# Optimization experiments

Measured on AMD Instinct MI355X. Metric: run time of the kernel, lower is better.

Reference implementation:

```python
import jax, jax.numpy as jnp
import numpy as np

HEADS = 16
DIM_HEAD = 64
NONCAUSAL_ATTN_LEN = 64


def setup_inputs() -> dict:
    key = jax.random.key(0)
    k1, k2, k3 = jax.random.split(key, 3)
    b, n, d = 2, 2048, 1024
    inner = HEADS * DIM_HEAD
    x = jax.random.normal(k1, (b, n, d), dtype=jnp.float32)
    mask = jnp.ones((b, n), dtype=bool)
    w_qkv = jax.random.normal(k2, (d, 3 * inner), dtype=jnp.float32) * 0.02
    w_out = jax.random.normal(k3, (inner, d), dtype=jnp.float32) * 0.02
    b_out = jnp.zeros((d,), dtype=jnp.float32)
    return {"x": x, "mask": mask, "w_qkv": w_qkv, "w_out": w_out, "b_out": b_out}


def reference(x, mask, w_qkv, w_out, b_out):
    b, n, _ = x.shape
    h, dh = HEADS, DIM_HEAD
    scale = dh ** -0.5
    qkv = x @ w_qkv                                  # [b, n, 3*h*dh]
    q, k, v = jnp.split(qkv, 3, axis=-1)
    # 'b n (h d) -> b h n d'
    reshape = lambda t: t.reshape(b, n, h, dh).transpose(0, 2, 1, 3)
    q, k, v = reshape(q), reshape(k), reshape(v)
    dots = jnp.einsum('bhid,bhjd->bhij', q, k) * scale  # [b,h,n,n]
    neg = -jnp.finfo(dots.dtype).max
    # padding mask: attend only where both query and key positions are valid
    pm = mask[:, None, :, None] & mask[:, None, None, :]
    dots = jnp.where(~pm, neg, dots)
    # causal mask (strict upper triangle), with noncausal prefix block unmasked
    cm = jnp.triu(jnp.ones((n, n), dtype=bool), k=1)
    L = NONCAUSAL_ATTN_LEN
    if L > 1:
        cm = cm.at[:L, :L].set(False)
    dots = jnp.where(cm, neg, dots)
    attn = jax.nn.softmax(dots, axis=-1)
    out = jnp.einsum('bhij,bhjd->bhid', attn, v)     # [b,h,n,dh]
    out = out.transpose(0, 2, 1, 3).reshape(b, n, h * dh)  # 'b h n d -> b n (h d)'
    return out @ w_out + b_out
```

## Files before the change

kernel.cpp:

```cpp
#include <hip/hip_runtime.h>

typedef __bf16 bf16x8 __attribute__((ext_vector_type(8)));
typedef __bf16 bf16x4 __attribute__((ext_vector_type(4)));
typedef float  f32x4  __attribute__((ext_vector_type(4)));

#define SC2 0.18033688011112042f

__device__ __forceinline__ void gload16(const void* g, void* l) {
    __builtin_amdgcn_global_load_lds(
        (const __attribute__((address_space(1))) unsigned int*)g,
        (__attribute__((address_space(3))) unsigned int*)l, 16, 0, 0);
}

__device__ __forceinline__ float max3f(float a, float b, float c) {
    return fmaxf(fmaxf(a, b), c);
}

__global__ __launch_bounds__(256) void prep_k(
    const float* __restrict__ x, const float* __restrict__ w_qkv,
    const float* __restrict__ w_out, __bf16* __restrict__ xb,
    __bf16* __restrict__ wqkvT, __bf16* __restrict__ woutT)
{
    __shared__ float tile[32][33];
    const int blk = blockIdx.x, tid = threadIdx.x;
    if (blk < 4096) {
        int i = blk * 256 + tid;
        float4 v = ((const float4*)x)[i];
        bf16x4 o;
        o[0] = (__bf16)v.x; o[1] = (__bf16)v.y; o[2] = (__bf16)v.z; o[3] = (__bf16)v.w;
        ((bf16x4*)xb)[i] = o;
        return;
    }
    const float* in; __bf16* outp; int C, t0;
    if (blk < 7168) { in = w_qkv; outp = wqkvT; C = 3072; t0 = blk - 4096; }
    else            { in = w_out; outp = woutT; C = 1024; t0 = blk - 7168; }
    const int R = 1024;
    const int tpr = C >> 5;
    const int c0 = (t0 % tpr) * 32, r0 = (t0 / tpr) * 32;
    const int tx = tid & 31, ty = tid >> 5;
#pragma unroll
    for (int p = 0; p < 4; ++p)
        tile[ty + p * 8][tx] = in[(size_t)(r0 + ty + p * 8) * C + c0 + tx];
    __syncthreads();
#pragma unroll
    for (int p = 0; p < 4; ++p)
        outp[(size_t)(c0 + ty + p * 8) * R + r0 + tx] = (__bf16)tile[tx][ty + p * 8];
}

template<int MODE, int BM>
__global__ __launch_bounds__(256) void gemm_bf16_k(
    const __bf16* __restrict__ A, const __bf16* __restrict__ Bt,
    void* __restrict__ Cout, const float* __restrict__ bias,
    int M, int N, int K)
{
    constexpr int MI = BM / 32;
    __shared__ __bf16 As[2][BM * 32];
    __shared__ __bf16 Bs[2][128 * 32];
    const int tid = threadIdx.x;
    const int m0 = blockIdx.x * BM, n0 = blockIdx.y * 128;
    const int wave = tid >> 6, lane = tid & 63;
    const int lr = lane & 15, lk = lane >> 4;

    const int row4 = lane >> 2;
    const int sg   = (lane & 3) ^ (row4 & 3);

    const int wm = (BM == 128) ? (wave >> 1) * 64 : (wave & 1) * 32;
    const int wn = (BM == 128) ? (wave & 1) * 64 : (wave >> 1) * 64;

    f32x4 acc[MI][4] = {};

    auto stage = [&](int k0, int bufi) {
        if (BM == 128) {
#pragma unroll
            for (int c = 0; c < 2; ++c) {
                int row = c * 64 + wave * 16 + row4;
                gload16(A + (size_t)(m0 + row) * K + k0 + sg * 8,
                        (char*)&As[bufi][0] + c * 4096 + wave * 1024);
            }
        } else {
            int row = wave * 16 + row4;
            gload16(A + (size_t)(m0 + row) * K + k0 + sg * 8,
                    (char*)&As[bufi][0] + wave * 1024);
        }
#pragma unroll
        for (int c = 0; c < 2; ++c) {
            int row = c * 64 + wave * 16 + row4;
            gload16(Bt + (size_t)(n0 + row) * K + k0 + sg * 8,
                    (char*)&Bs[bufi][0] + c * 4096 + wave * 1024);
        }
    };

    const int nsteps = K >> 5;
    stage(0, 0);
    for (int s = 0; s < nsteps; ++s) {
        __syncthreads();
        if (s + 1 < nsteps) stage((s + 1) * 32, (s + 1) & 1);
        const int bufi = s & 1;

        bf16x8 af[MI], bfr[4];
#pragma unroll
        for (int i = 0; i < MI; ++i) {
            int row = wm + i * 16 + lr;
            af[i]  = *(const bf16x8*)((char*)&As[bufi][0] + row * 64 +
                                      ((lk ^ (row & 3)) << 4));
        }
#pragma unroll
        for (int j = 0; j < 4; ++j) {
            int row = wn + j * 16 + lr;
            bfr[j] = *(const bf16x8*)((char*)&Bs[bufi][0] + row * 64 +
                                      ((lk ^ (row & 3)) << 4));
        }
        __builtin_amdgcn_s_setprio(1);
#pragma unroll
        for (int i = 0; i < MI; ++i)
#pragma unroll
            for (int j = 0; j < 4; ++j)
                acc[i][j] = __builtin_amdgcn_mfma_f32_16x16x32_bf16(
                    af[i], bfr[j], acc[i][j], 0, 0, 0);
        __builtin_amdgcn_s_setprio(0);
    }

#pragma unroll
    for (int i = 0; i < MI; ++i) {
#pragma unroll
        for (int j = 0; j < 4; ++j) {
            int row0 = m0 + wm + i * 16 + lk * 4;
            int col  = n0 + wn + j * 16 + lr;
            if (MODE == 0) {
                int which = col >> 10, rem = col & 1023;
                int h = rem >> 6, dh = rem & 63;
                int bb = row0 >> 11, nn0 = row0 & 2047;
                if (which == 2) {
                    bf16x4 o;
#pragma unroll
                    for (int r = 0; r < 4; ++r) o[r] = (__bf16)acc[i][j][r];
                    size_t off = (size_t)8388608 +
                                 (((size_t)bb * 16 + h) * 64 + dh) * 2048 + nn0;
                    *(bf16x4*)((__bf16*)Cout + off) = o;
                } else {
                    float sc = (which == 0) ? SC2 : 1.f;
#pragma unroll
                    for (int r = 0; r < 4; ++r) {
                        size_t off = ((((size_t)which * 2 + bb) * 16 + h) * 2048
                                      + nn0 + r) * 64 + dh;
                        ((__bf16*)Cout)[off] = (__bf16)(acc[i][j][r] * sc);
                    }
                }
            } else {
#pragma unroll
                for (int r = 0; r < 4; ++r)
                    ((float*)Cout)[(size_t)(row0 + r) * N + col] =
                        acc[i][j][r] + bias[col];
            }
        }
    }
}

__global__ __launch_bounds__(256) void flash_attn_k(
    const __bf16* __restrict__ qkv, __bf16* __restrict__ out)
{
    __shared__ __bf16 Ks[2][64 * 64];
    __shared__ __bf16 Vt[2][64 * 64];
    __shared__ __bf16 Ps[4 * 16 * 64];

    const int g = blockIdx.x;
    const int xcd = g & 7, i = g >> 3;
    const int bh = xcd + 8 * (i & 3);
    const int qp = i >> 2;
    const int qtA = qp, qtB = 31 - qp;
    const int b = bh >> 4, h = bh & 15;
    const int wave = threadIdx.x >> 6, lane = threadIdx.x & 63;
    const int lr = lane & 15, lk = lane >> 4;

    const size_t headoff = ((size_t)b * 16 + h) * 2048 * 64;
    const __bf16* Qp  = qkv + headoff;
    const __bf16* Kp  = qkv + (size_t)4194304 + headoff;
    const __bf16* Vtp = qkv + (size_t)8388608 + headoff;

    const int row8 = lane >> 3;
    const int sg   = (lane & 7) ^ row8;

    bf16x8 qfA[2], qfB[2];
    {
        const __bf16* qa = Qp + (size_t)(qtA * 64 + wave * 16 + lr) * 64 + lk * 8;
        qfA[0] = *(const bf16x8*)(qa);
        qfA[1] = *(const bf16x8*)(qa + 32);
        const __bf16* qb = Qp + (size_t)(qtB * 64 + wave * 16 + lr) * 64 + lk * 8;
        qfB[0] = *(const bf16x8*)(qb);
        qfB[1] = *(const bf16x8*)(qb + 32);
    }

    bf16x8 ones;
#pragma unroll
    for (int j = 0; j < 8; ++j) ones[j] = (__bf16)1.0f;

    float mA = 0.f, mB = 0.f;
    f32x4 lAacc = {}, lBacc = {};
    f32x4 oA[4] = {}, oB[4] = {};

    char* PsW = (char*)Ps + wave * 2048;

    auto stage = [&](int t, int bufi) {
        const int j0 = t * 64;
#pragma unroll
        for (int c = 0; c < 2; ++c) {
            int row = c * 32 + wave * 8 + row8;
            gload16(Kp + (size_t)(j0 + row) * 64 + sg * 8,
                    (char*)&Ks[bufi][0] + c * 4096 + wave * 1024);
            gload16(Vtp + (size_t)row * 2048 + j0 + sg * 8,
                    (char*)&Vt[bufi][0] + c * 4096 + wave * 1024);
        }
    };

    auto process = [&](int bufi, const bf16x8 (&qf)[2], float& m, f32x4& lacc,
                       f32x4 (&acc_o)[4], bool diag) {
        const float nm = -m;
        f32x4 sacc[4];
#pragma unroll
        for (int nf = 0; nf < 4; ++nf) sacc[nf] = f32x4{nm, nm, nm, nm};
        __builtin_amdgcn_s_setprio(1);
#pragma unroll
        for (int nf = 0; nf < 4; ++nf) {
            int arow = nf * 16 + lr;
#pragma unroll
            for (int ks = 0; ks < 2; ++ks) {
                int kb = (arow * 128 + (ks * 32 + lk * 8) * 2) ^ ((arow & 7) << 4);
                bf16x8 kf = *(const bf16x8*)((char*)&Ks[bufi][0] + kb);
                sacc[nf] = __builtin_amdgcn_mfma_f32_16x16x32_bf16(
                    kf, qf[ks], sacc[nf], 0, 0, 0);
            }
        }
        __builtin_amdgcn_s_setprio(0);
        if (diag) {
#pragma unroll
            for (int nf = 0; nf < 4; ++nf)
#pragma unroll
                for (int r = 0; r < 4; ++r)
                    if (nf * 16 + lk * 4 + r > wave * 16 + lr)
                        sacc[nf][r] = -1e30f;
        }
        float t0 = max3f(sacc[0][0], sacc[0][1], sacc[0][2]);
        float t1 = max3f(sacc[0][3], sacc[1][0], sacc[1][1]);
        float t2 = max3f(sacc[1][2], sacc[1][3], sacc[2][0]);
        float t3 = max3f(sacc[2][1], sacc[2][2], sacc[2][3]);
        float t4 = max3f(sacc[3][0], sacc[3][1], sacc[3][2]);
        float v = fmaxf(max3f(max3f(t0, t1, t2), t3, t4), sacc[3][3]);
        v = fmaxf(v, __shfl_xor(v, 16));
        v = fmaxf(v, __shfl_xor(v, 32));
        if (__builtin_expect(__any(v > 8.f), 0)) {
            float vc = fmaxf(v, 0.f);
            float alpha = exp2f(-vc);
            m += vc;
            float a_r[4];
#pragma unroll
            for (int r = 0; r < 4; ++r) a_r[r] = __shfl(alpha, lk * 4 + r);
#pragma unroll
            for (int r = 0; r < 4; ++r) lacc[r] *= a_r[r];
#pragma unroll
            for (int nf = 0; nf < 4; ++nf)
#pragma unroll
                for (int r = 0; r < 4; ++r) {
                    acc_o[nf][r] *= a_r[r];
                    sacc[nf][r] -= vc;
                }
        }
#pragma unroll
        for (int nf = 0; nf < 4; ++nf) {
            bf16x4 o;
#pragma unroll
            for (int r = 0; r < 4; ++r) o[r] = (__bf16)exp2f(sacc[nf][r]);
            int pb = (lr * 128 + nf * 32 + lk * 8) ^ ((lr & 7) << 4);
            *(bf16x4*)(PsW + pb) = o;
        }
        __builtin_amdgcn_s_setprio(1);
#pragma unroll
        for (int ks = 0; ks < 2; ++ks) {
            int pb = (lr * 128 + ks * 64 + lk * 16) ^ ((lr & 7) << 4);
            bf16x8 pa = *(const bf16x8*)(PsW + pb);
            lacc = __builtin_amdgcn_mfma_f32_16x16x32_bf16(pa, ones, lacc, 0, 0, 0);
#pragma unroll
            for (int nf = 0; nf < 4; ++nf) {
                int d = nf * 16 + lr;
                int vb = (d * 128 + ks * 64 + lk * 16) ^ ((d & 7) << 4);
                bf16x8 vf = *(const bf16x8*)((char*)&Vt[bufi][0] + vb);
                acc_o[nf] = __builtin_amdgcn_mfma_f32_16x16x32_bf16(
                    pa, vf, acc_o[nf], 0, 0, 0);
            }
        }
        __builtin_amdgcn_s_setprio(0);
    };

    const int nt = qtB + 1;
    stage(0, 0);
    for (int t = 0; t < nt; ++t) {
        __syncthreads();
        if (t + 1 < nt) stage(t + 1, (t + 1) & 1);
        if (t <= qtA) process(t & 1, qfA, mA, lAacc, oA, t == qtA && qtA > 0);
        process(t & 1, qfB, mB, lBacc, oB, t == qtB);
    }

    float lAr[4], lBr[4];
#pragma unroll
    for (int r = 0; r < 4; ++r) {
        lAr[r] = 1.f / lAacc[r];
        lBr[r] = 1.f / lBacc[r];
    }
    const int rowbase = (b << 11) + wave * 16 + lk * 4;
    const int colbase = h * 64 + lr;
#pragma unroll
    for (int nf = 0; nf < 4; ++nf)
#pragma unroll
        for (int r = 0; r < 4; ++r) {
            out[(size_t)(rowbase + qtA * 64 + r) * 1024 + colbase + nf * 16] =
                (__bf16)(oA[nf][r] * lAr[r]);
            out[(size_t)(rowbase + qtB * 64 + r) * 1024 + colbase + nf * 16] =
                (__bf16)(oB[nf][r] * lBr[r]);
        }
}

extern "C" void kernel_launch(void* const* d_in, const int* in_sizes, int n_in,
                              void* d_out, int out_size, void* d_ws, size_t ws_size,
                              hipStream_t stream)
{
    const float* x     = (const float*)d_in[0];
    const float* w_qkv = (const float*)d_in[2];
    const float* w_out = (const float*)d_in[3];
    const float* b_out = (const float*)d_in[4];

    char* ws = (char*)d_ws;
    __bf16* xb    = (__bf16*)(ws);
    __bf16* wqkvT = (__bf16*)(ws + 8388608);
    __bf16* woutT = (__bf16*)(ws + 14680064);
    __bf16* qkvp  = (__bf16*)(ws + 16777216);
    __bf16* aout  = (__bf16*)(ws + 41943040);

    prep_k<<<8192, 256, 0, stream>>>(x, w_qkv, w_out, xb, wqkvT, woutT);

    gemm_bf16_k<0, 128><<<dim3(32, 24), 256, 0, stream>>>(
        xb, wqkvT, (void*)qkvp, nullptr, 4096, 3072, 1024);
    flash_attn_k<<<512, 256, 0, stream>>>(qkvp, aout);
    gemm_bf16_k<1, 64><<<dim3(64, 8), 256, 0, stream>>>(
        aout, woutT, (void*)d_out, b_out, 4096, 1024, 1024);
}
```

Measured before the change: 113.1 us.

## Rewrite flash attention with 32x32 MFMA, 2-wave blocks, one query tile each

The attention kernel moves from 16x16x32 to 32x32x16 bf16 MFMA, with each of two waves owning 32 query rows. Blocks shrink from 256 to 128 threads, and each block now handles a single query tile instead of a paired short/long tile, so the grid doubles to 1024. The goal is fewer MFMA issues and fewer LDS fragment reads per unit of work, and more blocks for the scheduler to spread. In exchange, the paired-tile load balancing is gone, and the row rescale now goes through an LDS round trip instead of shuffles.

```diff
diff --git a/kernel.cpp b/kernel.cpp
--- a/kernel.cpp
+++ b/kernel.cpp
@@ -3,6 +3,7 @@
 typedef __bf16 bf16x8 __attribute__((ext_vector_type(8)));
 typedef __bf16 bf16x4 __attribute__((ext_vector_type(4)));
 typedef float  f32x4  __attribute__((ext_vector_type(4)));
+typedef float  f32x16 __attribute__((ext_vector_type(16)));
 
 #define SC2 0.18033688011112042f
 
@@ -156,166 +157,158 @@
     }
 }
 
-__global__ __launch_bounds__(256) void flash_attn_k(
+__global__ __launch_bounds__(128) void flash_attn_k(
     const __bf16* __restrict__ qkv, __bf16* __restrict__ out)
 {
     __shared__ __bf16 Ks[2][64 * 64];
     __shared__ __bf16 Vt[2][64 * 64];
-    __shared__ __bf16 Ps[4 * 16 * 64];
+    __shared__ __bf16 Ps[2][32 * 64];
 
     const int g = blockIdx.x;
     const int xcd = g & 7, i = g >> 3;
     const int bh = xcd + 8 * (i & 3);
-    const int qp = i >> 2;
-    const int qtA = qp, qtB = 31 - qp;
-    const int b = bh >> 4, h = bh & 15;
+    const int qt = 31 - (i >> 2);
+    const int b = bh >> 4, hh = bh & 15;
     const int wave = threadIdx.x >> 6, lane = threadIdx.x & 63;
-    const int lr = lane & 15, lk = lane >> 4;
-
-    const size_t headoff = ((size_t)b * 16 + h) * 2048 * 64;
+    const int l31 = lane & 31, lh = lane >> 5;
+
+    const size_t headoff = ((size_t)b * 16 + hh) * 2048 * 64;
     const __bf16* Qp  = qkv + headoff;
     const __bf16* Kp  = qkv + (size_t)4194304 + headoff;
     const __bf16* Vtp = qkv + (size_t)8388608 + headoff;
 
     const int row8 = lane >> 3;
     const int sg   = (lane & 7) ^ row8;
-
-    bf16x8 qfA[2], qfB[2];
+    const int swz  = (l31 & 7) << 4;
+
+    bf16x8 qf[4];
     {
-        const __bf16* qa = Qp + (size_t)(qtA * 64 + wave * 16 + lr) * 64 + lk * 8;
-        qfA[0] = *(const bf16x8*)(qa);
-        qfA[1] = *(const bf16x8*)(qa + 32);
-        const __bf16* qb = Qp + (size_t)(qtB * 64 + wave * 16 + lr) * 64 + lk * 8;
-        qfB[0] = *(const bf16x8*)(qb);
-        qfB[1] = *(const bf16x8*)(qb + 32);
+        const __bf16* qa = Qp + (size_t)(qt * 64 + wave * 32 + l31) * 64 + lh * 8;
+#pragma unroll
+        for (int ks = 0; ks < 4; ++ks) qf[ks] = *(const bf16x8*)(qa + ks * 16);
     }
 
     bf16x8 ones;
 #pragma unroll
     for (int j = 0; j < 8; ++j) ones[j] = (__bf16)1.0f;
 
-    float mA = 0.f, mB = 0.f;
-    f32x4 lAacc = {}, lBacc = {};
-    f32x4 oA[4] = {}, oB[4] = {};
-
-    char* PsW = (char*)Ps + wave * 2048;
+    float m = 0.f;
+    f32x16 lacc = {};
+    f32x16 o0 = {}, o1 = {};
+
+    char* PsW = (char*)&Ps[wave][0];
 
     auto stage = [&](int t, int bufi) {
         const int j0 = t * 64;
 #pragma unroll
-        for (int c = 0; c < 2; ++c) {
-            int row = c * 32 + wave * 8 + row8;
+        for (int c = 0; c < 4; ++c) {
+            int row = c * 16 + wave * 8 + row8;
             gload16(Kp + (size_t)(j0 + row) * 64 + sg * 8,
-                    (char*)&Ks[bufi][0] + c * 4096 + wave * 1024);
+                    (char*)&Ks[bufi][0] + c * 2048 + wave * 1024);
             gload16(Vtp + (size_t)row * 2048 + j0 + sg * 8,
-                    (char*)&Vt[bufi][0] + c * 4096 + wave * 1024);
+                    (char*)&Vt[bufi][0] + c * 2048 + wave * 1024);
         }
     };
 
-    auto process = [&](int bufi, const bf16x8 (&qf)[2], float& m, f32x4& lacc,
-                       f32x4 (&acc_o)[4], bool diag) {
+    const int nt = qt + 1;
+    stage(0, 0);
+    for (int t = 0; t < nt; ++t) {
+        __syncthreads();
+        if (t + 1 < nt) stage(t + 1, (t + 1) & 1);
+        const int bufi = t & 1;
+
         const float nm = -m;
-        f32x4 sacc[4];
-#pragma unroll
-        for (int nf = 0; nf < 4; ++nf) sacc[nf] = f32x4{nm, nm, nm, nm};
+        f32x16 s0, s1;
+#pragma unroll
+        for (int r = 0; r < 16; ++r) { s0[r] = nm; s1[r] = nm; }
         __builtin_amdgcn_s_setprio(1);
 #pragma unroll
-        for (int nf = 0; nf < 4; ++nf) {
-            int arow = nf * 16 + lr;
-#pragma unroll
-            for (int ks = 0; ks < 2; ++ks) {
-                int kb = (arow * 128 + (ks * 32 + lk * 8) * 2) ^ ((arow & 7) << 4);
-                bf16x8 kf = *(const bf16x8*)((char*)&Ks[bufi][0] + kb);
-                sacc[nf] = __builtin_amdgcn_mfma_f32_16x16x32_bf16(
-                    kf, qf[ks], sacc[nf], 0, 0, 0);
-            }
+        for (int ks = 0; ks < 4; ++ks) {
+            int kb = l31 * 128 + ((ks * 32 + lh * 16) ^ swz);
+            bf16x8 kf0 = *(const bf16x8*)((char*)&Ks[bufi][0] + kb);
+            bf16x8 kf1 = *(const bf16x8*)((char*)&Ks[bufi][0] + kb + 4096);
+            s0 = __builtin_amdgcn_mfma_f32_32x32x16_bf16(kf0, qf[ks], s0, 0, 0, 0);
+            s1 = __builtin_amdgcn_mfma_f32_32x32x16_bf16(kf1, qf[ks], s1, 0, 0, 0);
         }
         __builtin_amdgcn_s_setprio(0);
-        if (diag) {
-#pragma unroll
-            for (int nf = 0; nf < 4; ++nf)
-#pragma unroll
-                for (int r = 0; r < 4; ++r)
-                    if (nf * 16 + lk * 4 + r > wave * 16 + lr)
-                        sacc[nf][r] = -1e30f;
-        }
-        float t0 = max3f(sacc[0][0], sacc[0][1], sacc[0][2]);
-        float t1 = max3f(sacc[0][3], sacc[1][0], sacc[1][1]);
-        float t2 = max3f(sacc[1][2], sacc[1][3], sacc[2][0]);
-        float t3 = max3f(sacc[2][1], sacc[2][2], sacc[2][3]);
-        float t4 = max3f(sacc[3][0], sacc[3][1], sacc[3][2]);
-        float v = fmaxf(max3f(max3f(t0, t1, t2), t3, t4), sacc[3][3]);
-        v = fmaxf(v, __shfl_xor(v, 16));
+
+        if (t == qt && qt > 0) {
+            int q = wave * 32 + l31;
+#pragma unroll
+            for (int r = 0; r < 16; ++r) {
+                int key = (r & 3) + 8 * (r >> 2) + 4 * lh;
+                if (key > q)      s0[r] = -1e30f;
+                if (key + 32 > q) s1[r] = -1e30f;
+            }
+        }
+
+        float a0 = max3f(s0[0], s0[1], s0[2]);
+        float a1 = max3f(s0[3], s0[4], s0[5]);
+        float a2 = max3f(s0[6], s0[7], s0[8]);
+        float a3 = max3f(s0[9], s0[10], s0[11]);
+        float a4 = max3f(s0[12], s0[13], s0[14]);
+        float a5 = max3f(s0[15], s1[0], s1[1]);
+        float a6 = max3f(s1[2], s1[3], s1[4]);
+        float a7 = max3f(s1[5], s1[6], s1[7]);
+        float a8 = max3f(s1[8], s1[9], s1[10]);
+        float a9 = max3f(s1[11], s1[12], s1[13]);
+        float aa = fmaxf(s1[14], s1[15]);
+        float v  = max3f(max3f(a0, a1, a2), max3f(a3, a4, a5),
+                         max3f(a6, a7, a8));
+        v = max3f(v, a9, aa);
         v = fmaxf(v, __shfl_xor(v, 32));
+
         if (__builtin_expect(__any(v > 8.f), 0)) {
             float vc = fmaxf(v, 0.f);
             float alpha = exp2f(-vc);
             m += vc;
-            float a_r[4];
-#pragma unroll
-            for (int r = 0; r < 4; ++r) a_r[r] = __shfl(alpha, lk * 4 + r);
-#pragma unroll
-            for (int r = 0; r < 4; ++r) lacc[r] *= a_r[r];
-#pragma unroll
-            for (int nf = 0; nf < 4; ++nf)
-#pragma unroll
-                for (int r = 0; r < 4; ++r) {
-                    acc_o[nf][r] *= a_r[r];
-                    sacc[nf][r] -= vc;
-                }
-        }
-#pragma unroll
-        for (int nf = 0; nf < 4; ++nf) {
-            bf16x4 o;
-#pragma unroll
-            for (int r = 0; r < 4; ++r) o[r] = (__bf16)exp2f(sacc[nf][r]);
-            int pb = (lr * 128 + nf * 32 + lk * 8) ^ ((lr & 7) << 4);
-            *(bf16x4*)(PsW + pb) = o;
-        }
+            *(float*)(PsW + l31 * 4) = alpha;
+            float ar[16];
+#pragma unroll
+            for (int r = 0; r < 16; ++r)
+                ar[r] = *(float*)(PsW + ((r & 3) + 8 * (r >> 2) + 4 * lh) * 4);
+#pragma unroll
+            for (int r = 0; r < 16; ++r) {
+                o0[r] *= ar[r]; o1[r] *= ar[r]; lacc[r] *= ar[r];
+                s0[r] -= vc;    s1[r] -= vc;
+            }
+        }
+
+#pragma unroll
+        for (int gp = 0; gp < 4; ++gp) {
+            bf16x4 p0, p1;
+#pragma unroll
+            for (int r = 0; r < 4; ++r) {
+                p0[r] = (__bf16)exp2f(s0[gp * 4 + r]);
+                p1[r] = (__bf16)exp2f(s1[gp * 4 + r]);
+            }
+            *(bf16x4*)(PsW + l31 * 128 + ((16 * gp + 8 * lh) ^ swz)) = p0;
+            *(bf16x4*)(PsW + l31 * 128 + ((64 + 16 * gp + 8 * lh) ^ swz)) = p1;
+        }
+
         __builtin_amdgcn_s_setprio(1);
 #pragma unroll
-        for (int ks = 0; ks < 2; ++ks) {
-            int pb = (lr * 128 + ks * 64 + lk * 16) ^ ((lr & 7) << 4);
-            bf16x8 pa = *(const bf16x8*)(PsW + pb);
-            lacc = __builtin_amdgcn_mfma_f32_16x16x32_bf16(pa, ones, lacc, 0, 0, 0);
-#pragma unroll
-            for (int nf = 0; nf < 4; ++nf) {
-                int d = nf * 16 + lr;
-                int vb = (d * 128 + ks * 64 + lk * 16) ^ ((d & 7) << 4);
-                bf16x8 vf = *(const bf16x8*)((char*)&Vt[bufi][0] + vb);
-                acc_o[nf] = __builtin_amdgcn_mfma_f32_16x16x32_bf16(
-                    pa, vf, acc_o[nf], 0, 0, 0);
-            }
+        for (int s = 0; s < 4; ++s) {
+            int po = l31 * 128 + ((s * 32 + lh * 16) ^ swz);
+            bf16x8 paf = *(const bf16x8*)(PsW + po);
+            lacc = __builtin_amdgcn_mfma_f32_32x32x16_bf16(paf, ones, lacc, 0, 0, 0);
+            bf16x8 vf0 = *(const bf16x8*)((char*)&Vt[bufi][0] + po);
+            bf16x8 vf1 = *(const bf16x8*)((char*)&Vt[bufi][0] + po + 4096);
+            o0 = __builtin_amdgcn_mfma_f32_32x32x16_bf16(paf, vf0, o0, 0, 0, 0);
+            o1 = __builtin_amdgcn_mfma_f32_32x32x16_bf16(paf, vf1, o1, 0, 0, 0);
         }
         __builtin_amdgcn_s_setprio(0);
-    };
-
-    const int nt = qtB + 1;
-    stage(0, 0);
-    for (int t = 0; t < nt; ++t) {
-        __syncthreads();
-        if (t + 1 < nt) stage(t + 1, (t + 1) & 1);
-        if (t <= qtA) process(t & 1, qfA, mA, lAacc, oA, t == qtA && qtA > 0);
-        process(t & 1, qfB, mB, lBacc, oB, t == qtB);
-    }
-
-    float lAr[4], lBr[4];
-#pragma unroll
-    for (int r = 0; r < 4; ++r) {
-        lAr[r] = 1.f / lAacc[r];
-        lBr[r] = 1.f / lBacc[r];
-    }
-    const int rowbase = (b << 11) + wave * 16 + lk * 4;
-    const int colbase = h * 64 + lr;
-#pragma unroll
-    for (int nf = 0; nf < 4; ++nf)
-#pragma unroll
-        for (int r = 0; r < 4; ++r) {
-            out[(size_t)(rowbase + qtA * 64 + r) * 1024 + colbase + nf * 16] =
-                (__bf16)(oA[nf][r] * lAr[r]);
-            out[(size_t)(rowbase + qtB * 64 + r) * 1024 + colbase + nf * 16] =
-                (__bf16)(oB[nf][r] * lBr[r]);
-        }
+    }
+
+    const int rowbase = (b << 11) + qt * 64 + wave * 32;
+    const int colbase = hh * 64 + l31;
+#pragma unroll
+    for (int r = 0; r < 16; ++r) {
+        float linv = 1.f / lacc[r];
+        int q = (r & 3) + 8 * (r >> 2) + 4 * lh;
+        out[(size_t)(rowbase + q) * 1024 + colbase]      = (__bf16)(o0[r] * linv);
+        out[(size_t)(rowbase + q) * 1024 + colbase + 32] = (__bf16)(o1[r] * linv);
+    }
 }
 
 extern "C" void kernel_launch(void* const* d_in, const int* in_sizes, int n_in,
@@ -338,7 +331,7 @@
 
     gemm_bf16_k<0, 128><<<dim3(32, 24), 256, 0, stream>>>(
         xb, wqkvT, (void*)qkvp, nullptr, 4096, 3072, 1024);
-    flash_attn_k<<<512, 256, 0, stream>>>(qkvp, aout);
+    flash_attn_k<<<1024, 128, 0, stream>>>(qkvp, aout);
     gemm_bf16_k<1, 64><<<dim3(64, 8), 256, 0, stream>>>(
         aout, woutT, (void*)d_out, b_out, 4096, 1024, 1024);
 }
```

New measurement: 126.1 us. 11.5% more time.

## Fuse paired query tiles per K/V step and reorder block-to-tile mapping

Applied to the files above, without the earlier changes.

While both query tiles are active, the attention loop now computes them together in a single fused step. Each K and V fragment read from LDS feeds two MFMAs, and the two softmax chains are interleaved to expose more independent work. The P staging buffer is doubled so each tile has its own region. Block indices are also remapped so that adjacent blocks take mirrored query-pair indices, which is meant to even out per-block work across the grid. The cost is more LDS and more register pressure from the doubled accumulators, which could reduce occupancy.

```diff
diff --git a/kernel.cpp b/kernel.cpp
--- a/kernel.cpp
+++ b/kernel.cpp
@@ -161,12 +161,14 @@
 {
     __shared__ __bf16 Ks[2][64 * 64];
     __shared__ __bf16 Vt[2][64 * 64];
-    __shared__ __bf16 Ps[4 * 16 * 64];
+    __shared__ __bf16 Ps[4 * 2 * 16 * 64];
 
     const int g = blockIdx.x;
-    const int xcd = g & 7, i = g >> 3;
-    const int bh = xcd + 8 * (i & 3);
-    const int qp = i >> 2;
+    const int xcd = g & 7, ii = g >> 3;
+    const int pp = ii >> 1, e = ii & 1;
+    const int bh = xcd + 8 * (pp & 3);
+    const int rr = pp >> 2;
+    const int qp = e ? 15 - rr : rr;
     const int qtA = qp, qtB = 31 - qp;
     const int b = bh >> 4, h = bh & 15;
     const int wave = threadIdx.x >> 6, lane = threadIdx.x & 63;
@@ -198,7 +200,7 @@
     f32x4 lAacc = {}, lBacc = {};
     f32x4 oA[4] = {}, oB[4] = {};
 
-    char* PsW = (char*)Ps + wave * 2048;
+    char* PsW = (char*)Ps + wave * 4096;
 
     auto stage = [&](int t, int bufi) {
         const int j0 = t * 64;
@@ -212,25 +214,8 @@
         }
     };
 
-    auto process = [&](int bufi, const bf16x8 (&qf)[2], float& m, f32x4& lacc,
-                       f32x4 (&acc_o)[4], bool diag) {
-        const float nm = -m;
-        f32x4 sacc[4];
-#pragma unroll
-        for (int nf = 0; nf < 4; ++nf) sacc[nf] = f32x4{nm, nm, nm, nm};
-        __builtin_amdgcn_s_setprio(1);
-#pragma unroll
-        for (int nf = 0; nf < 4; ++nf) {
-            int arow = nf * 16 + lr;
-#pragma unroll
-            for (int ks = 0; ks < 2; ++ks) {
-                int kb = (arow * 128 + (ks * 32 + lk * 8) * 2) ^ ((arow & 7) << 4);
-                bf16x8 kf = *(const bf16x8*)((char*)&Ks[bufi][0] + kb);
-                sacc[nf] = __builtin_amdgcn_mfma_f32_16x16x32_bf16(
-                    kf, qf[ks], sacc[nf], 0, 0, 0);
-            }
-        }
-        __builtin_amdgcn_s_setprio(0);
+    auto softpart = [&](f32x4 (&sacc)[4], float& m, f32x4& lacc,
+                        f32x4 (&acc_o)[4], int psoff, bool diag) {
         if (diag) {
 #pragma unroll
             for (int nf = 0; nf < 4; ++nf)
@@ -270,33 +255,104 @@
 #pragma unroll
             for (int r = 0; r < 4; ++r) o[r] = (__bf16)exp2f(sacc[nf][r]);
             int pb = (lr * 128 + nf * 32 + lk * 8) ^ ((lr & 7) << 4);
-            *(bf16x4*)(PsW + pb) = o;
-        }
+            *(bf16x4*)(PsW + psoff + pb) = o;
+        }
+    };
+
+    auto process = [&](int bufi, bool diag) {
+        const float nm = -mB;
+        f32x4 sacc[4];
+#pragma unroll
+        for (int nf = 0; nf < 4; ++nf) sacc[nf] = f32x4{nm, nm, nm, nm};
+        __builtin_amdgcn_s_setprio(1);
+#pragma unroll
+        for (int nf = 0; nf < 4; ++nf) {
+            int arow = nf * 16 + lr;
+#pragma unroll
+            for (int ks = 0; ks < 2; ++ks) {
+                int kb = (arow * 128 + (ks * 32 + lk * 8) * 2) ^ ((arow & 7) << 4);
+                bf16x8 kf = *(const bf16x8*)((char*)&Ks[bufi][0] + kb);
+                sacc[nf] = __builtin_amdgcn_mfma_f32_16x16x32_bf16(
+                    kf, qfB[ks], sacc[nf], 0, 0, 0);
+            }
+        }
+        __builtin_amdgcn_s_setprio(0);
+        softpart(sacc, mB, lBacc, oB, 2048, diag);
         __builtin_amdgcn_s_setprio(1);
 #pragma unroll
         for (int ks = 0; ks < 2; ++ks) {
             int pb = (lr * 128 + ks * 64 + lk * 16) ^ ((lr & 7) << 4);
-            bf16x8 pa = *(const bf16x8*)(PsW + pb);
-            lacc = __builtin_amdgcn_mfma_f32_16x16x32_bf16(pa, ones, lacc, 0, 0, 0);
+            bf16x8 pa = *(const bf16x8*)(PsW + 2048 + pb);
+            lBacc = __builtin_amdgcn_mfma_f32_16x16x32_bf16(pa, ones, lBacc, 0, 0, 0);
 #pragma unroll
             for (int nf = 0; nf < 4; ++nf) {
                 int d = nf * 16 + lr;
                 int vb = (d * 128 + ks * 64 + lk * 16) ^ ((d & 7) << 4);
                 bf16x8 vf = *(const bf16x8*)((char*)&Vt[bufi][0] + vb);
-                acc_o[nf] = __builtin_amdgcn_mfma_f32_16x16x32_bf16(
-                    pa, vf, acc_o[nf], 0, 0, 0);
+                oB[nf] = __builtin_amdgcn_mfma_f32_16x16x32_bf16(
+                    pa, vf, oB[nf], 0, 0, 0);
             }
         }
         __builtin_amdgcn_s_setprio(0);
     };
 
-    const int nt = qtB + 1;
+    auto fused = [&](int bufi, bool diagA) {
+        const float nmA = -mA, nmB = -mB;
+        f32x4 sA[4], sB[4];
+#pragma unroll
+        for (int nf = 0; nf < 4; ++nf) {
+            sA[nf] = f32x4{nmA, nmA, nmA, nmA};
+            sB[nf] = f32x4{nmB, nmB, nmB, nmB};
+        }
+        __builtin_amdgcn_s_setprio(1);
+#pragma unroll
+        for (int nf = 0; nf < 4; ++nf) {
+            int arow = nf * 16 + lr;
+#pragma unroll
+            for (int ks = 0; ks < 2; ++ks) {
+                int kb = (arow * 128 + (ks * 32 + lk * 8) * 2) ^ ((arow & 7) << 4);
+                bf16x8 kf = *(const bf16x8*)((char*)&Ks[bufi][0] + kb);
+                sA[nf] = __builtin_amdgcn_mfma_f32_16x16x32_bf16(
+                    kf, qfA[ks], sA[nf], 0, 0, 0);
+                sB[nf] = __builtin_amdgcn_mfma_f32_16x16x32_bf16(
+                    kf, qfB[ks], sB[nf], 0, 0, 0);
+            }
+        }
+        __builtin_amdgcn_s_setprio(0);
+        softpart(sA, mA, lAacc, oA, 0, diagA);
+        softpart(sB, mB, lBacc, oB, 2048, false);
+        __builtin_amdgcn_s_setprio(1);
+#pragma unroll
+        for (int ks = 0; ks < 2; ++ks) {
+            int pb = (lr * 128 + ks * 64 + lk * 16) ^ ((lr & 7) << 4);
+            bf16x8 paA = *(const bf16x8*)(PsW + pb);
+            bf16x8 paB = *(const bf16x8*)(PsW + 2048 + pb);
+            lAacc = __builtin_amdgcn_mfma_f32_16x16x32_bf16(paA, ones, lAacc, 0, 0, 0);
+            lBacc = __builtin_amdgcn_mfma_f32_16x16x32_bf16(paB, ones, lBacc, 0, 0, 0);
+#pragma unroll
+            for (int nf = 0; nf < 4; ++nf) {
+                int d = nf * 16 + lr;
+                int vb = (d * 128 + ks * 64 + lk * 16) ^ ((d & 7) << 4);
+                bf16x8 vf = *(const bf16x8*)((char*)&Vt[bufi][0] + vb);
+                oA[nf] = __builtin_amdgcn_mfma_f32_16x16x32_bf16(
+                    paA, vf, oA[nf], 0, 0, 0);
+                oB[nf] = __builtin_amdgcn_mfma_f32_16x16x32_bf16(
+                    paB, vf, oB[nf], 0, 0, 0);
+            }
+        }
+        __builtin_amdgcn_s_setprio(0);
+    };
+
     stage(0, 0);
-    for (int t = 0; t < nt; ++t) {
+    for (int t = 0; t <= qtA; ++t) {
         __syncthreads();
-        if (t + 1 < nt) stage(t + 1, (t + 1) & 1);
-        if (t <= qtA) process(t & 1, qfA, mA, lAacc, oA, t == qtA && qtA > 0);
-        process(t & 1, qfB, mB, lBacc, oB, t == qtB);
+        if (t + 1 <= qtB) stage(t + 1, (t + 1) & 1);
+        fused(t & 1, t == qtA && qtA > 0);
+    }
+    for (int t = qtA + 1; t <= qtB; ++t) {
+        __syncthreads();
+        if (t + 1 <= qtB) stage(t + 1, (t + 1) & 1);
+        process(t & 1, t == qtB);
     }
 
     float lAr[4], lBr[4];
```

Result: no change. 112.7 us (-0.4%).
